# Kernel optimization log

Hardware: AMD Instinct MI355X
Metric: run time of the kernel (lower is better)

Reference implementation:

```python
import jax, jax.numpy as jnp
import numpy as np

INPUT_DIM = 512
OUTPUT_DIM = 512
DEGREE = 8
BATCH = 16384


def setup_inputs() -> dict:
    key = jax.random.key(0)
    kx, kc = jax.random.split(key)
    x = jax.random.normal(kx, (BATCH, INPUT_DIM), dtype=jnp.float32)
    cheby_coeffs = jax.random.normal(kc, (INPUT_DIM, OUTPUT_DIM, DEGREE + 1), dtype=jnp.float32) / jnp.sqrt(
        jnp.float32(INPUT_DIM * (DEGREE + 1))
    )
    return {"x": x, "cheby_coeffs": cheby_coeffs}


def reference(x, cheby_coeffs):
    degree = cheby_coeffs.shape[-1] - 1
    arange = jnp.arange(degree + 1, dtype=x.dtype)  # [d]
    t = jnp.tanh(x)  # [b, i], squash into [-1, 1]
    theta = jnp.arccos(t)[..., None] * arange  # [b, i, d]
    basis = jnp.cos(theta)  # Chebyshev T_n(tanh(x)) = cos(n * arccos(tanh(x)))
    y = jnp.einsum('bid,iod->bo', basis, cheby_coeffs)
    return y
```

## Files before the change

kernel.cpp:

```cpp
#include <hip/hip_runtime.h>
#include <hip/hip_bf16.h>
#include <stdint.h>


#define BM 128
#define BN 128
#define BK 32
#define NSTEPS 128
#define IN_DIM 512
#define OUT_DIM 512

typedef __attribute__((ext_vector_type(8))) short short8;
typedef __attribute__((ext_vector_type(8))) unsigned short ushort8;
typedef __attribute__((ext_vector_type(4))) float f32x4;

__device__ __forceinline__ unsigned short f2bf(float f) {
  __hip_bfloat16 h = __float2bfloat16(f);
  return __builtin_bit_cast(unsigned short, h);
}

__device__ __forceinline__ float fast_tanh(float v) {
  float e = __expf(v + v);
  return 1.0f - 2.0f * __builtin_amdgcn_rcpf(e + 1.0f);
}

__device__ __forceinline__ void gload_lds16(const void* g, void* l) {
  __builtin_amdgcn_global_load_lds(
      (const __attribute__((address_space(1))) unsigned int*)(uintptr_t)g,
      (__attribute__((address_space(3))) unsigned int*)(uintptr_t)l,
      16, 0, 0);
}

__global__ __launch_bounds__(256) void cheby_reorder_b(
    const float* __restrict__ coeffs, unsigned char* __restrict__ bws) {
  const int g = blockIdx.x * 256 + threadIdx.x;
  const int i = g & 511;
  const int o = g >> 9;
  const int nb = o >> 7, nl = o & 127;
  const int itile = i >> 5, kl = i & 31;
  const float* cp = coeffs + (size_t)i * 4608 + (size_t)o * 9;
  const int swz = ((kl * 2) ^ ((nl & 3) << 4));
#pragma unroll
  for (int d = 1; d <= 8; ++d) {
    const int c = itile * 8 + (d - 1);
    const size_t byte = ((size_t)(nb * 128 + c) << 13) + (size_t)nl * 64 + swz;
    *(unsigned short*)(bws + byte) = f2bf(cp[d]);
  }
}

__global__ __launch_bounds__(64) void cheby_colsum(
    const float* __restrict__ coeffs, float* __restrict__ cs) {
  const int o = blockIdx.x;
  const int l = threadIdx.x;
  float s = 0.0f;
#pragma unroll
  for (int j = 0; j < 8; ++j)
    s += coeffs[(size_t)(l + j * 64) * 4608 + (size_t)o * 9];
#pragma unroll
  for (int off = 32; off > 0; off >>= 1) s += __shfl_down(s, off, 64);
  if (l == 0) cs[o] = s;
}

__global__ __launch_bounds__(256, 2) void cheby_gemm(
    const float* __restrict__ x, const unsigned char* __restrict__ bws,
    const float* __restrict__ colsum, float* __restrict__ out) {
  const int bid = blockIdx.x;
  const int m0 = (bid >> 2) * BM;
  const int nblk = bid & 3;
  const int n0 = nblk * BN;
  const int tid = threadIdx.x;
  const int lane = tid & 63;
  const int wid = tid >> 6;
  const int wm = (wid >> 1) * 64;
  const int wn = (wid & 1) * 64;
  const int l15 = lane & 15;
  const int lhi = lane >> 4;

  __shared__ __align__(16) unsigned char As[BM * BK * 2];
  __shared__ __align__(16) unsigned char Bs[BN * BK * 2];

  const int srow = tid >> 1;
  const int skb = (tid & 1) * 32;
  unsigned char* Arow = As + srow * 64;
  const int sw0 = (skb) ^ ((srow & 3) << 4);
  const int sw1 = (skb + 16) ^ ((srow & 3) << 4);

  float t2[16], Tm1[16], Tm2[16];
  f32x4 acc[4][4];
#pragma unroll
  for (int a = 0; a < 4; ++a)
#pragma unroll
    for (int b = 0; b < 4; ++b) acc[a][b] = (f32x4){0.f, 0.f, 0.f, 0.f};

  const unsigned char* bchunk0 = bws + ((size_t)(nblk * 128) << 13);

  for (int s = 0; s < NSTEPS; ++s) {
    const unsigned char* gsrc =
        bchunk0 + ((size_t)s << 13) + wid * 1024 + lane * 16;
    gload_lds16(gsrc, Bs + wid * 1024);
    gload_lds16(gsrc + 4096, Bs + wid * 1024 + 4096);

    const int dd = s & 7;
    if (dd == 0) {
      const int itile = s >> 3;
      const float* xp =
          x + (size_t)(m0 + srow) * IN_DIM + itile * 32 + (tid & 1) * 16;
#pragma unroll
      for (int j = 0; j < 4; ++j) {
        const float4 v = reinterpret_cast<const float4*>(xp)[j];
        const float a0 = fast_tanh(v.x);
        const float a1 = fast_tanh(v.y);
        const float a2 = fast_tanh(v.z);
        const float a3 = fast_tanh(v.w);
        Tm1[4 * j + 0] = a0; Tm1[4 * j + 1] = a1;
        Tm1[4 * j + 2] = a2; Tm1[4 * j + 3] = a3;
        t2[4 * j + 0] = a0 + a0; t2[4 * j + 1] = a1 + a1;
        t2[4 * j + 2] = a2 + a2; t2[4 * j + 3] = a3 + a3;
        Tm2[4 * j + 0] = 1.0f; Tm2[4 * j + 1] = 1.0f;
        Tm2[4 * j + 2] = 1.0f; Tm2[4 * j + 3] = 1.0f;
      }
    } else {
#pragma unroll
      for (int e = 0; e < 16; ++e) {
        const float T = __builtin_fmaf(t2[e], Tm1[e], -Tm2[e]);
        Tm2[e] = Tm1[e];
        Tm1[e] = T;
      }
    }
    ushort8 p0, p1;
#pragma unroll
    for (int j = 0; j < 8; ++j) {
      p0[j] = f2bf(Tm1[j]);
      p1[j] = f2bf(Tm1[j + 8]);
    }
    *(ushort8*)(Arow + sw0) = p0;
    *(ushort8*)(Arow + sw1) = p1;

    __syncthreads();

    short8 af[4], bfr[4];
#pragma unroll
    for (int fm = 0; fm < 4; ++fm) {
      const int row = wm + fm * 16 + l15;
      af[fm] = *(const short8*)(As + row * 64 + ((lhi * 16) ^ ((row & 3) << 4)));
    }
#pragma unroll
    for (int fn = 0; fn < 4; ++fn) {
      const int row = wn + fn * 16 + l15;
      bfr[fn] = *(const short8*)(Bs + row * 64 + ((lhi * 16) ^ ((row & 3) << 4)));
    }
#pragma unroll
    for (int fm = 0; fm < 4; ++fm)
#pragma unroll
      for (int fn = 0; fn < 4; ++fn)
        acc[fm][fn] = __builtin_amdgcn_mfma_f32_16x16x32_bf16(
            af[fm], bfr[fn], acc[fm][fn], 0, 0, 0);

    __syncthreads();
  }

  float csv[4];
#pragma unroll
  for (int fn = 0; fn < 4; ++fn) csv[fn] = colsum[n0 + wn + fn * 16 + l15];
#pragma unroll
  for (int fm = 0; fm < 4; ++fm) {
    const int r0 = m0 + wm + fm * 16 + lhi * 4;
#pragma unroll
    for (int fn = 0; fn < 4; ++fn) {
      const int col = n0 + wn + fn * 16 + l15;
#pragma unroll
      for (int r = 0; r < 4; ++r)
        out[(size_t)(r0 + r) * OUT_DIM + col] = acc[fm][fn][r] + csv[fn];
    }
  }
}

extern "C" void kernel_launch(void* const* d_in, const int* in_sizes, int n_in,
                              void* d_out, int out_size, void* d_ws,
                              size_t ws_size, hipStream_t stream) {
  const float* x = (const float*)d_in[0];
  const float* coeffs = (const float*)d_in[1];
  float* out = (float*)d_out;
  unsigned char* bws = (unsigned char*)d_ws;
  float* cs = (float*)((unsigned char*)d_ws + ((size_t)4 << 20));

  hipLaunchKernelGGL(cheby_reorder_b, dim3(1024), dim3(256), 0, stream, coeffs,
                     bws);
  hipLaunchKernelGGL(cheby_colsum, dim3(512), dim3(64), 0, stream, coeffs, cs);
  hipLaunchKernelGGL(cheby_gemm, dim3(512), dim3(256), 0, stream, x, bws, cs,
                     out);
}
```

Before: 119.3 us.

## Double K-tile to 64 by packing two Chebyshev degrees per step

Each main-loop step now covers two Chebyshev degrees (K=64) instead of one, which halves the number of loop iterations and barrier pairs. The recurrence advances two terms per step, and the reordered B layout and LDS swizzle are widened to 128-byte rows to match. Launch bounds move from 2 to 3 blocks per SM, trading register budget for occupancy. LDS per block doubles, and the tighter register cap risks spills.

New measurement: 97.53 us. 18.2% less time.

```diff
diff --git a/kernel.cpp b/kernel.cpp
--- a/kernel.cpp
+++ b/kernel.cpp
@@ -5,8 +5,8 @@
 
 #define BM 128
 #define BN 128
-#define BK 32
-#define NSTEPS 128
+#define BK 64
+#define NSTEPS 64
 #define IN_DIM 512
 #define OUT_DIM 512
 
@@ -37,14 +37,16 @@
   const int i = g & 511;
   const int o = g >> 9;
   const int nb = o >> 7, nl = o & 127;
-  const int itile = i >> 5, kl = i & 31;
+  const int itile = i >> 5, il = i & 31;
   const float* cp = coeffs + (size_t)i * 4608 + (size_t)o * 9;
-  const int swz = ((kl * 2) ^ ((nl & 3) << 4));
-#pragma unroll
-  for (int d = 1; d <= 8; ++d) {
-    const int c = itile * 8 + (d - 1);
-    const size_t byte = ((size_t)(nb * 128 + c) << 13) + (size_t)nl * 64 + swz;
-    *(unsigned short*)(bws + byte) = f2bf(cp[d]);
+  const int swz = (nl & 7) << 4;
+#pragma unroll
+  for (int p = 0; p < 4; ++p) {
+    const size_t base =
+        ((size_t)(nb * 64 + itile * 4 + p) << 14) + (size_t)nl * 128;
+    *(unsigned short*)(bws + base + ((il * 2) ^ swz)) = f2bf(cp[1 + 2 * p]);
+    *(unsigned short*)(bws + base + ((64 + il * 2) ^ swz)) =
+        f2bf(cp[2 + 2 * p]);
   }
 }
 
@@ -61,7 +63,7 @@
   if (l == 0) cs[o] = s;
 }
 
-__global__ __launch_bounds__(256, 2) void cheby_gemm(
+__global__ __launch_bounds__(256, 3) void cheby_gemm(
     const float* __restrict__ x, const unsigned char* __restrict__ bws,
     const float* __restrict__ colsum, float* __restrict__ out) {
   const int bid = blockIdx.x;
@@ -76,14 +78,14 @@
   const int l15 = lane & 15;
   const int lhi = lane >> 4;
 
-  __shared__ __align__(16) unsigned char As[BM * BK * 2];
-  __shared__ __align__(16) unsigned char Bs[BN * BK * 2];
+  __shared__ __align__(16) unsigned char As[BM * 128];
+  __shared__ __align__(16) unsigned char Bs[BN * 128];
 
   const int srow = tid >> 1;
-  const int skb = (tid & 1) * 32;
-  unsigned char* Arow = As + srow * 64;
-  const int sw0 = (skb) ^ ((srow & 3) << 4);
-  const int sw1 = (skb + 16) ^ ((srow & 3) << 4);
+  const int ihalf = tid & 1;
+  unsigned char* Arow = As + srow * 128;
+  const int aswz = (srow & 7) << 4;
+  const int wbase = ihalf * 32;
 
   float t2[16], Tm1[16], Tm2[16];
   f32x4 acc[4][4];
@@ -92,19 +94,22 @@
 #pragma unroll
     for (int b = 0; b < 4; ++b) acc[a][b] = (f32x4){0.f, 0.f, 0.f, 0.f};
 
-  const unsigned char* bchunk0 = bws + ((size_t)(nblk * 128) << 13);
+  const unsigned char* bchunk0 = bws + ((size_t)(nblk * 64) << 14);
 
   for (int s = 0; s < NSTEPS; ++s) {
     const unsigned char* gsrc =
-        bchunk0 + ((size_t)s << 13) + wid * 1024 + lane * 16;
-    gload_lds16(gsrc, Bs + wid * 1024);
-    gload_lds16(gsrc + 4096, Bs + wid * 1024 + 4096);
-
-    const int dd = s & 7;
-    if (dd == 0) {
-      const int itile = s >> 3;
+        bchunk0 + ((size_t)s << 14) + wid * 4096 + lane * 16;
+    unsigned char* ldst = Bs + wid * 4096;
+    gload_lds16(gsrc, ldst);
+    gload_lds16(gsrc + 1024, ldst + 1024);
+    gload_lds16(gsrc + 2048, ldst + 2048);
+    gload_lds16(gsrc + 3072, ldst + 3072);
+
+    const int p = s & 3;
+    if (p == 0) {
+      const int itile = s >> 2;
       const float* xp =
-          x + (size_t)(m0 + srow) * IN_DIM + itile * 32 + (tid & 1) * 16;
+          x + (size_t)(m0 + srow) * IN_DIM + itile * 32 + ihalf * 16;
 #pragma unroll
       for (int j = 0; j < 4; ++j) {
         const float4 v = reinterpret_cast<const float4*>(xp)[j];
@@ -112,50 +117,59 @@
         const float a1 = fast_tanh(v.y);
         const float a2 = fast_tanh(v.z);
         const float a3 = fast_tanh(v.w);
-        Tm1[4 * j + 0] = a0; Tm1[4 * j + 1] = a1;
-        Tm1[4 * j + 2] = a2; Tm1[4 * j + 3] = a3;
+        Tm2[4 * j + 0] = a0; Tm2[4 * j + 1] = a1;
+        Tm2[4 * j + 2] = a2; Tm2[4 * j + 3] = a3;
         t2[4 * j + 0] = a0 + a0; t2[4 * j + 1] = a1 + a1;
         t2[4 * j + 2] = a2 + a2; t2[4 * j + 3] = a3 + a3;
-        Tm2[4 * j + 0] = 1.0f; Tm2[4 * j + 1] = 1.0f;
-        Tm2[4 * j + 2] = 1.0f; Tm2[4 * j + 3] = 1.0f;
+        Tm1[4 * j + 0] = __builtin_fmaf(a0 + a0, a0, -1.0f);
+        Tm1[4 * j + 1] = __builtin_fmaf(a1 + a1, a1, -1.0f);
+        Tm1[4 * j + 2] = __builtin_fmaf(a2 + a2, a2, -1.0f);
+        Tm1[4 * j + 3] = __builtin_fmaf(a3 + a3, a3, -1.0f);
       }
     } else {
 #pragma unroll
       for (int e = 0; e < 16; ++e) {
-        const float T = __builtin_fmaf(t2[e], Tm1[e], -Tm2[e]);
-        Tm2[e] = Tm1[e];
-        Tm1[e] = T;
-      }
-    }
-    ushort8 p0, p1;
+        const float Ta = __builtin_fmaf(t2[e], Tm1[e], -Tm2[e]);
+        const float Tb = __builtin_fmaf(t2[e], Ta, -Tm1[e]);
+        Tm2[e] = Ta;
+        Tm1[e] = Tb;
+      }
+    }
+    ushort8 pa0, pa1, pb0, pb1;
 #pragma unroll
     for (int j = 0; j < 8; ++j) {
-      p0[j] = f2bf(Tm1[j]);
-      p1[j] = f2bf(Tm1[j + 8]);
-    }
-    *(ushort8*)(Arow + sw0) = p0;
-    *(ushort8*)(Arow + sw1) = p1;
+      pa0[j] = f2bf(Tm2[j]);
+      pa1[j] = f2bf(Tm2[j + 8]);
+      pb0[j] = f2bf(Tm1[j]);
+      pb1[j] = f2bf(Tm1[j + 8]);
+    }
+    *(ushort8*)(Arow + ((wbase) ^ aswz)) = pa0;
+    *(ushort8*)(Arow + ((wbase + 16) ^ aswz)) = pa1;
+    *(ushort8*)(Arow + ((64 + wbase) ^ aswz)) = pb0;
+    *(ushort8*)(Arow + ((64 + wbase + 16) ^ aswz)) = pb1;
 
     __syncthreads();
 
-    short8 af[4], bfr[4];
-#pragma unroll
-    for (int fm = 0; fm < 4; ++fm) {
-      const int row = wm + fm * 16 + l15;
-      af[fm] = *(const short8*)(As + row * 64 + ((lhi * 16) ^ ((row & 3) << 4)));
-    }
-#pragma unroll
-    for (int fn = 0; fn < 4; ++fn) {
-      const int row = wn + fn * 16 + l15;
-      bfr[fn] = *(const short8*)(Bs + row * 64 + ((lhi * 16) ^ ((row & 3) << 4)));
-    }
-#pragma unroll
-    for (int fm = 0; fm < 4; ++fm)
-#pragma unroll
-      for (int fn = 0; fn < 4; ++fn)
-        acc[fm][fn] = __builtin_amdgcn_mfma_f32_16x16x32_bf16(
-            af[fm], bfr[fn], acc[fm][fn], 0, 0, 0);
-
+#pragma unroll
+    for (int ks = 0; ks < 2; ++ks) {
+      short8 af[4];
+#pragma unroll
+      for (int fm = 0; fm < 4; ++fm) {
+        const int row = wm + fm * 16 + l15;
+        af[fm] = *(const short8*)(
+            As + row * 128 + ((ks * 64 + lhi * 16) ^ ((row & 7) << 4)));
+      }
+#pragma unroll
+      for (int fn = 0; fn < 4; ++fn) {
+        const int row = wn + fn * 16 + l15;
+        const short8 bf = *(const short8*)(
+            Bs + row * 128 + ((ks * 64 + lhi * 16) ^ ((row & 7) << 4)));
+#pragma unroll
+        for (int fm = 0; fm < 4; ++fm)
+          acc[fm][fn] = __builtin_amdgcn_mfma_f32_16x16x32_bf16(
+              af[fm], bf, acc[fm][fn], 0, 0, 0);
+      }
+    }
     __syncthreads();
   }
 
```

## Drop LDS staging; per-wave register-resident Chebyshev GEMM with double-buffered B fragments

Applied to the files above, without the earlier changes.

Each wave now owns an independent 32x64 output tile. It builds the Chebyshev A fragments directly in registers in MFMA layout and loads B fragments straight from global memory into registers, double-buffered across steps. This removes the shared-memory tiles, the swizzled LDS writes and reads, and both __syncthreads per k-step. The B reorder kernel writes a new layout matched to the fragment loads, and the grid doubles to 1024 blocks. The cost is far less data reuse per wave: B is re-read from global/L2 by many more waves, and register pressure goes up.

After: 279.3 us. 134% more time.

```diff
diff --git a/kernel.cpp b/kernel.cpp
--- a/kernel.cpp
+++ b/kernel.cpp
@@ -3,15 +3,10 @@
 #include <stdint.h>
 
 
-#define BM 128
-#define BN 128
-#define BK 32
-#define NSTEPS 128
 #define IN_DIM 512
 #define OUT_DIM 512
 
 typedef __attribute__((ext_vector_type(8))) short short8;
-typedef __attribute__((ext_vector_type(8))) unsigned short ushort8;
 typedef __attribute__((ext_vector_type(4))) float f32x4;
 
 __device__ __forceinline__ unsigned short f2bf(float f) {
@@ -24,27 +19,19 @@
   return 1.0f - 2.0f * __builtin_amdgcn_rcpf(e + 1.0f);
 }
 
-__device__ __forceinline__ void gload_lds16(const void* g, void* l) {
-  __builtin_amdgcn_global_load_lds(
-      (const __attribute__((address_space(1))) unsigned int*)(uintptr_t)g,
-      (__attribute__((address_space(3))) unsigned int*)(uintptr_t)l,
-      16, 0, 0);
-}
-
 __global__ __launch_bounds__(256) void cheby_reorder_b(
     const float* __restrict__ coeffs, unsigned char* __restrict__ bws) {
   const int g = blockIdx.x * 256 + threadIdx.x;
   const int i = g & 511;
   const int o = g >> 9;
-  const int nb = o >> 7, nl = o & 127;
-  const int itile = i >> 5, kl = i & 31;
+  const int it = i >> 5, il = i & 31;
   const float* cp = coeffs + (size_t)i * 4608 + (size_t)o * 9;
-  const int swz = ((kl * 2) ^ ((nl & 3) << 4));
 #pragma unroll
-  for (int d = 1; d <= 8; ++d) {
-    const int c = itile * 8 + (d - 1);
-    const size_t byte = ((size_t)(nb * 128 + c) << 13) + (size_t)nl * 64 + swz;
-    *(unsigned short*)(bws + byte) = f2bf(cp[d]);
+  for (int p = 0; p < 4; ++p) {
+    unsigned char* base =
+        bws + (((size_t)(it * 4 + p)) << 16) + (size_t)o * 128 + il * 2;
+    *(unsigned short*)(base) = f2bf(cp[1 + 2 * p]);
+    *(unsigned short*)(base + 64) = f2bf(cp[2 + 2 * p]);
   }
 }
 
@@ -61,113 +48,121 @@
   if (l == 0) cs[o] = s;
 }
 
+#define ISSUE_BF(S, BUF)                                                   \
+  {                                                                        \
+    const unsigned char* bs = bbase + ((size_t)(S) << 16);                 \
+    _Pragma("unroll") for (int fn = 0; fn < 4; ++fn)                       \
+        _Pragma("unroll") for (int ks = 0; ks < 2; ++ks)                   \
+            BUF[fn][ks] =                                                  \
+                *(const short8*)(bs + fn * 2048 + ks * 64);                \
+  }
+
+#define MFMA8(AF, BUF, KS)                                                 \
+  {                                                                        \
+    _Pragma("unroll") for (int fn = 0; fn < 4; ++fn)                       \
+        _Pragma("unroll") for (int fm = 0; fm < 2; ++fm)                   \
+            acc[fm][fn] = __builtin_amdgcn_mfma_f32_16x16x32_bf16(         \
+                AF[fm], BUF[fn][KS], acc[fm][fn], 0, 0, 0);                \
+  }
+
+#define GEN_A()                                                            \
+  {                                                                        \
+    _Pragma("unroll") for (int fm = 0; fm < 2; ++fm)                       \
+        _Pragma("unroll") for (int j = 0; j < 8; ++j) {                    \
+      Tpp[fm][j] = __builtin_fmaf(t2[fm][j], Tp[fm][j], -Tpp[fm][j]);      \
+      af1[fm][j] = (short)f2bf(Tpp[fm][j]);                                \
+    }                                                                      \
+  }
+
+#define GEN_B()                                                            \
+  {                                                                        \
+    _Pragma("unroll") for (int fm = 0; fm < 2; ++fm)                       \
+        _Pragma("unroll") for (int j = 0; j < 8; ++j) {                    \
+      Tp[fm][j] = __builtin_fmaf(t2[fm][j], Tpp[fm][j], -Tp[fm][j]);       \
+      afC[fm][j] = (short)f2bf(Tp[fm][j]);                                 \
+    }                                                                      \
+  }
+
+#define INIT_()                                                            \
+  {                                                                        \
+    _Pragma("unroll") for (int fm = 0; fm < 2; ++fm)                       \
+        _Pragma("unroll") for (int j = 0; j < 8; ++j) {                    \
+      const float xval = ((const float*)&xv[fm][j >> 2])[j & 3];           \
+      const float th = fast_tanh(xval);                                    \
+      t2[fm][j] = th + th;                                                 \
+      Tp[fm][j] = th;                                                      \
+      Tpp[fm][j] = 1.0f;                                                   \
+      afC[fm][j] = (short)f2bf(th);                                        \
+    }                                                                      \
+  }
+
+#define LOAD_X(IT)                                                         \
+  {                                                                        \
+    xv[0][0] = reinterpret_cast<const float4*>(xr0 + (IT) * 32)[0];        \
+    xv[0][1] = reinterpret_cast<const float4*>(xr0 + (IT) * 32)[1];        \
+    xv[1][0] = reinterpret_cast<const float4*>(xr1 + (IT) * 32)[0];        \
+    xv[1][1] = reinterpret_cast<const float4*>(xr1 + (IT) * 32)[1];        \
+  }
+
+#define STEP(IT, Q, BUFC, BUFN)                                            \
+  {                                                                        \
+    const int s_ = (IT) * 4 + (Q);                                         \
+    if ((Q) == 2) LOAD_X(((IT) < 15) ? (IT) + 1 : 15);                     \
+    ISSUE_BF((s_ < 63) ? s_ + 1 : 63, BUFN);                               \
+    __builtin_amdgcn_sched_barrier(0);                                     \
+    MFMA8(afC, BUFC, 0);                            \
+    GEN_A();                                       \
+    MFMA8(af1, BUFC, 1);                            \
+    if ((Q) == 3) { INIT_(); } else { GEN_B(); }    \
+  }
+
 __global__ __launch_bounds__(256, 2) void cheby_gemm(
     const float* __restrict__ x, const unsigned char* __restrict__ bws,
     const float* __restrict__ colsum, float* __restrict__ out) {
-  const int bid = blockIdx.x;
-  const int m0 = (bid >> 2) * BM;
-  const int nblk = bid & 3;
-  const int n0 = nblk * BN;
-  const int tid = threadIdx.x;
-  const int lane = tid & 63;
-  const int wid = tid >> 6;
-  const int wm = (wid >> 1) * 64;
-  const int wn = (wid & 1) * 64;
+  const int gwid = blockIdx.x * 4 + (threadIdx.x >> 6);
+  const int lane = threadIdx.x & 63;
   const int l15 = lane & 15;
   const int lhi = lane >> 4;
+  const int nblk = gwid >> 9;
+  const int m0 = (gwid & 511) * 32;
+  const int n0 = nblk * 64;
 
-  __shared__ __align__(16) unsigned char As[BM * BK * 2];
-  __shared__ __align__(16) unsigned char Bs[BN * BK * 2];
+  const float* xr0 = x + (size_t)(m0 + l15) * IN_DIM + lhi * 8;
+  const float* xr1 = xr0 + (size_t)16 * IN_DIM;
+  const unsigned char* bbase =
+      bws + (size_t)(n0 + l15) * 128 + lhi * 16;
 
-  const int srow = tid >> 1;
-  const int skb = (tid & 1) * 32;
-  unsigned char* Arow = As + srow * 64;
-  const int sw0 = (skb) ^ ((srow & 3) << 4);
-  const int sw1 = (skb + 16) ^ ((srow & 3) << 4);
-
-  float t2[16], Tm1[16], Tm2[16];
-  f32x4 acc[4][4];
+  float t2[2][8], Tp[2][8], Tpp[2][8];
+  short8 afC[2], af1[2];
+  short8 bfE[4][2], bfO[4][2];
+  float4 xv[2][2];
+  f32x4 acc[2][4];
 #pragma unroll
-  for (int a = 0; a < 4; ++a)
+  for (int a = 0; a < 2; ++a)
 #pragma unroll
     for (int b = 0; b < 4; ++b) acc[a][b] = (f32x4){0.f, 0.f, 0.f, 0.f};
 
-  const unsigned char* bchunk0 = bws + ((size_t)(nblk * 128) << 13);
+  LOAD_X(0);
+  ISSUE_BF(0, bfE);
+  INIT_();
 
-  for (int s = 0; s < NSTEPS; ++s) {
-    const unsigned char* gsrc =
-        bchunk0 + ((size_t)s << 13) + wid * 1024 + lane * 16;
-    gload_lds16(gsrc, Bs + wid * 1024);
-    gload_lds16(gsrc + 4096, Bs + wid * 1024 + 4096);
-
-    const int dd = s & 7;
-    if (dd == 0) {
-      const int itile = s >> 3;
-      const float* xp =
-          x + (size_t)(m0 + srow) * IN_DIM + itile * 32 + (tid & 1) * 16;
-#pragma unroll
-      for (int j = 0; j < 4; ++j) {
-        const float4 v = reinterpret_cast<const float4*>(xp)[j];
-        const float a0 = fast_tanh(v.x);
-        const float a1 = fast_tanh(v.y);
-        const float a2 = fast_tanh(v.z);
-        const float a3 = fast_tanh(v.w);
-        Tm1[4 * j + 0] = a0; Tm1[4 * j + 1] = a1;
-        Tm1[4 * j + 2] = a2; Tm1[4 * j + 3] = a3;
-        t2[4 * j + 0] = a0 + a0; t2[4 * j + 1] = a1 + a1;
-        t2[4 * j + 2] = a2 + a2; t2[4 * j + 3] = a3 + a3;
-        Tm2[4 * j + 0] = 1.0f; Tm2[4 * j + 1] = 1.0f;
-        Tm2[4 * j + 2] = 1.0f; Tm2[4 * j + 3] = 1.0f;
-      }
-    } else {
-#pragma unroll
-      for (int e = 0; e < 16; ++e) {
-        const float T = __builtin_fmaf(t2[e], Tm1[e], -Tm2[e]);
-        Tm2[e] = Tm1[e];
-        Tm1[e] = T;
-      }
-    }
-    ushort8 p0, p1;
-#pragma unroll
-    for (int j = 0; j < 8; ++j) {
-      p0[j] = f2bf(Tm1[j]);
-      p1[j] = f2bf(Tm1[j + 8]);
-    }
-    *(ushort8*)(Arow + sw0) = p0;
-    *(ushort8*)(Arow + sw1) = p1;
-
-    __syncthreads();
-
-    short8 af[4], bfr[4];
-#pragma unroll
-    for (int fm = 0; fm < 4; ++fm) {
-      const int row = wm + fm * 16 + l15;
-      af[fm] = *(const short8*)(As + row * 64 + ((lhi * 16) ^ ((row & 3) << 4)));
-    }
-#pragma unroll
-    for (int fn = 0; fn < 4; ++fn) {
-      const int row = wn + fn * 16 + l15;
-      bfr[fn] = *(const short8*)(Bs + row * 64 + ((lhi * 16) ^ ((row & 3) << 4)));
-    }
-#pragma unroll
-    for (int fm = 0; fm < 4; ++fm)
-#pragma unroll
-      for (int fn = 0; fn < 4; ++fn)
-        acc[fm][fn] = __builtin_amdgcn_mfma_f32_16x16x32_bf16(
-            af[fm], bfr[fn], acc[fm][fn], 0, 0, 0);
-
-    __syncthreads();
+  for (int it = 0; it < 16; ++it) {
+    STEP(it, 0, bfE, bfO);
+    STEP(it, 1, bfO, bfE);
+    STEP(it, 2, bfE, bfO);
+    STEP(it, 3, bfO, bfE);
   }
 
   float csv[4];
 #pragma unroll
-  for (int fn = 0; fn < 4; ++fn) csv[fn] = colsum[n0 + wn + fn * 16 + l15];
+  for (int fn = 0; fn < 4; ++fn) csv[fn] = colsum[n0 + fn * 16 + l15];
+  const int lhi4 = lhi * 4;
 #pragma unroll
-  for (int fm = 0; fm < 4; ++fm) {
-    const int r0 = m0 + wm + fm * 16 + lhi * 4;
+  for (int fm = 0; fm < 2; ++fm) {
+    const int r0 = m0 + fm * 16 + lhi4;
 #pragma unroll
     for (int fn = 0; fn < 4; ++fn) {
-      const int col = n0 + wn + fn * 16 + l15;
+      const int col = n0 + fn * 16 + l15;
 #pragma unroll
       for (int r = 0; r < 4; ++r)
         out[(size_t)(r0 + r) * OUT_DIM + col] = acc[fm][fn][r] + csv[fn];
@@ -187,6 +182,6 @@
   hipLaunchKernelGGL(cheby_reorder_b, dim3(1024), dim3(256), 0, stream, coeffs,
                      bws);
   hipLaunchKernelGGL(cheby_colsum, dim3(512), dim3(64), 0, stream, coeffs, cs);
-  hipLaunchKernelGGL(cheby_gemm, dim3(512), dim3(256), 0, stream, x, bws, cs,
+  hipLaunchKernelGGL(cheby_gemm, dim3(1024), dim3(256), 0, stream, x, bws, cs,
                      out);
 }
```
